# Kernel optimization log

Hardware: AMD Instinct MI355X
Metric: run time of the kernel (lower is better)

Reference implementation:

```python
import jax, jax.numpy as jnp
import numpy as np

CONF_THRESHOLD = 4.0
NMS_THRESHOLD = 0.5
TOP_K = 4096        # fixed candidate cap for jit-static shapes (>> expected #candidates)
NEG = -1.0e9


def setup_inputs() -> dict:
    key = jax.random.key(0)
    k1, k2, k3 = jax.random.split(key, 3)
    B, N, C = 8, 65536, 80
    logits = jax.random.normal(k1, (B, N, C), dtype=jnp.float32)
    # valid xyxy boxes in a ~1000px image: x2>x1, y2>y1
    xy = jax.random.uniform(k2, (B, N, 2), dtype=jnp.float32) * 900.0
    wh = jax.random.uniform(k3, (B, N, 2), dtype=jnp.float32) * 100.0 + 1.0
    boxes = jnp.concatenate([xy, xy + wh], axis=-1)
    return {"logits": logits, "boxes": boxes}


def _pairwise_iou(b):
    # b: [K, 4] xyxy -> [K, K] IoU (torchvision convention, no +1)
    x1, y1, x2, y2 = b[:, 0], b[:, 1], b[:, 2], b[:, 3]
    area = (x2 - x1) * (y2 - y1)                      # [K]
    iw = jnp.maximum(jnp.minimum(x2[:, None], x2[None, :]) - jnp.maximum(x1[:, None], x1[None, :]), 0.0)
    ih = jnp.maximum(jnp.minimum(y2[:, None], y2[None, :]) - jnp.maximum(y1[:, None], y1[None, :]), 0.0)
    inter = iw * ih                                   # [K, K]
    union = area[:, None] + area[None, :] - inter
    return inter / jnp.maximum(union, 1e-12)


def reference(logits, boxes):
    B, N, C = logits.shape
    scores = jnp.max(logits, axis=2)                  # [B, N]
    cls = jnp.argmax(logits, axis=2)                  # [B, N]
    # per-(image, class) NMS category id, as in the torch module
    cat = cls + jnp.arange(B, dtype=cls.dtype)[:, None] * C
    valid = scores > CONF_THRESHOLD                   # [B, N]
    img = jnp.broadcast_to(jnp.arange(B, dtype=jnp.int32)[:, None], (B, N))

    scores_f = scores.reshape(-1)
    valid_f = valid.reshape(-1)
    boxes_f = boxes.reshape(-1, 4)
    cat_f = cat.reshape(-1)
    cls_f = cls.reshape(-1)
    img_f = img.reshape(-1)

    # global descending-score order (matches batched_nms sort); invalid pushed to bottom
    vals, idx = jax.lax.top_k(jnp.where(valid_f, scores_f, NEG), TOP_K)
    bx = boxes_f[idx]                                 # [K, 4]
    ct = cat_f[idx]
    cl = cls_f[idx]
    im = img_f[idx]
    vk = valid_f[idx]                                 # [K]

    iou = _pairwise_iou(bx)                           # [K, K]
    suppress_mat = (ct[:, None] == ct[None, :]) & (iou > NMS_THRESHOLD)
    order = jnp.arange(TOP_K)

    def body(i, keep):
        sup = suppress_mat[i] & (order > i)
        return jnp.where(keep[i], keep & ~sup, keep)

    keep = jax.lax.fori_loop(0, TOP_K, body, vk)      # greedy NMS suppression

    nms_image_idx = jnp.where(keep, im, -1)
    nms_bboxes = bx * keep[:, None].astype(bx.dtype)
    nms_classes = jnp.where(keep, cl, -1)
    nms_scores = jnp.where(keep, vals, 0.0)
    return (nms_image_idx, nms_bboxes, nms_classes, nms_scores)
```

## Files before the change

kernel.cpp:

```cpp
#include <hip/hip_runtime.h>
#include <stdint.h>

typedef unsigned long long u64;
typedef unsigned int u32;
typedef float fv4 __attribute__((ext_vector_type(4)));

#define BATCH  8
#define NPTS   65536
#define NCLS   80
#define NANCH  (BATCH * NPTS)
#define TOPK   4096
#define CONF   4.0f
#define NMSTH  0.5f
#define NCAT   (BATCH * NCLS)
#define BCAP   32

static constexpr size_t OFF_CNT  = 0;
static constexpr size_t OFF_KEYS = 64;

__global__ __launch_bounds__(64) void k_score(const float* __restrict__ logits,
                                              int* __restrict__ cnt,
                                              u64* __restrict__ keys) {
    __shared__ u32 s_sc[64 * 21];
    __shared__ unsigned char s_cl[64 * 20];
    int lane = threadIdx.x;
    const fv4* src = (const fv4*)logits + (size_t)blockIdx.x * 1280;
#pragma unroll
    for (int k = 0; k < 20; ++k) {
        int e = k * 64 + lane;
        fv4 v = __builtin_nontemporal_load(&src[e]);
        float bv = v.x; int bc = 0;
        if (v.y > bv) { bv = v.y; bc = 1; }
        if (v.z > bv) { bv = v.z; bc = 2; }
        if (v.w > bv) { bv = v.w; bc = 3; }
        int a_l = e / 20, j = e % 20;
        u32 eb = __float_as_uint(bv);
        eb = (eb & 0x80000000u) ? ~eb : (eb | 0x80000000u);
        s_sc[a_l * 21 + j] = eb;
        s_cl[a_l * 20 + j] = (unsigned char)(j * 4 + bc);
    }
    __syncthreads();
    u32 best = 0; int bj = 0;
#pragma unroll
    for (int j = 0; j < 20; ++j) {
        u32 p = s_sc[lane * 21 + j];
        if (p > best) { best = p; bj = j; }
    }
    u32 orig = (best & 0x80000000u) ? (best & 0x7fffffffu) : ~best;
    if (__uint_as_float(orig) > CONF) {
        u32 cls = s_cl[lane * 20 + bj];
        u32 a = blockIdx.x * 64 + (u32)lane;
        int pos = atomicAdd(cnt, 1);
        if (pos < 8192)
            keys[pos] = ((u64)best << 32) | ((((~a) & 0x7FFFFu) << 7) | cls);
    }
}

__global__ __launch_bounds__(1024) void k_nms(const int* __restrict__ cnt,
                                              const u64* __restrict__ keys_raw,
                                              const float* __restrict__ boxes,
                                              float* __restrict__ out) {
    __shared__ u64    s_keys[4096];
    __shared__ float4 s_box[4096];
    __shared__ unsigned short s_bucket[NCAT * BCAP];
    __shared__ int s_bcnt[NCAT];
    __shared__ unsigned char s_keep[4096];
    int n = min(*cnt, TOPK);
    int tid = threadIdx.x;
    int n2 = 64; while (n2 < n) n2 <<= 1;

    for (int c = tid; c < NCAT; c += 1024) s_bcnt[c] = 0;
    for (int i = tid; i < n2; i += 1024)
        s_keys[i] = (i < n) ? keys_raw[i] : 0ull;
    __syncthreads();

    for (int k = 2; k <= n2; k <<= 1) {
        for (int j = k >> 1; j > 0; j >>= 1) {
            for (int i = tid; i < n2; i += 1024) {
                int ixj = i ^ j;
                if (ixj > i) {
                    u64 x = s_keys[i], y = s_keys[ixj];
                    bool desc = ((i & k) == 0);
                    if (desc ? (x < y) : (x > y)) { s_keys[i] = y; s_keys[ixj] = x; }
                }
            }
            __syncthreads();
        }
    }

    float4 bx[4]; int cls_[4], img_[4]; float sc_[4];
#pragma unroll
    for (int r = 0; r < 4; ++r) {
        int s = tid + 1024 * r;
        float4 b = make_float4(0.f, 0.f, 0.f, 0.f);
        int cl = -1, im = -1; float v = 0.f;
        if (s < n) {
            u64 key = s_keys[s];
            u32 eb = (u32)(key >> 32);
            u32 orig = (eb & 0x80000000u) ? (eb & 0x7fffffffu) : ~eb;
            v = __uint_as_float(orig);
            u32 low = (u32)key;
            cl = (int)(low & 0x7fu);
            u32 a = (~(low >> 7)) & 0x7FFFFu;
            im = (int)(a >> 16);
            b = ((const float4*)boxes)[a];
            int c = im * NCLS + cl;
            int pos = atomicAdd(&s_bcnt[c], 1);
            if (pos < BCAP) s_bucket[c * BCAP + pos] = (unsigned short)s;
        }
        bx[r] = b; cls_[r] = cl; img_[r] = im; sc_[r] = v;
        s_box[s]  = b;
        s_keep[s] = (s < n) ? 1 : 0;
    }
    __syncthreads();

    if (tid < NCAT) {
        int m = min(s_bcnt[tid], BCAP);
        unsigned short* bkt = &s_bucket[tid * BCAP];
        if (m > 1) {
            for (int i = 1; i < m; ++i) {
                unsigned short x = bkt[i]; int j = i - 1;
                while (j >= 0 && bkt[j] > x) { bkt[j + 1] = bkt[j]; --j; }
                bkt[j + 1] = x;
            }
            for (int i = 1; i < m; ++i) {
                float4 bi = s_box[bkt[i]];
                float areai = (bi.z - bi.x) * (bi.w - bi.y);
                bool dead = false;
                for (int j = 0; j < i && !dead; ++j) {
                    if (!s_keep[bkt[j]]) continue;
                    float4 bj = s_box[bkt[j]];
                    float iw = fmaxf(fminf(bi.z, bj.z) - fmaxf(bi.x, bj.x), 0.f);
                    float ih = fmaxf(fminf(bi.w, bj.w) - fmaxf(bi.y, bj.y), 0.f);
                    float inter = iw * ih;
                    float uni = areai + (bj.z - bj.x) * (bj.w - bj.y) - inter;
                    if (inter / fmaxf(uni, 1e-12f) > NMSTH) dead = true;
                }
                if (dead) s_keep[bkt[i]] = 0;
            }
        }
    }
    __syncthreads();

#pragma unroll
    for (int r = 0; r < 4; ++r) {
        int s = tid + 1024 * r;
        bool keep = s_keep[s] != 0;
        out[s] = keep ? (float)img_[r] : -1.0f;
        ((float4*)(out + 4096))[s] = keep ? bx[r] : make_float4(0.f, 0.f, 0.f, 0.f);
        out[4096 + 16384 + s]        = keep ? (float)cls_[r] : -1.0f;
        out[4096 + 16384 + 4096 + s] = keep ? sc_[r] : 0.0f;
    }
}

extern "C" void kernel_launch(void* const* d_in, const int* in_sizes, int n_in,
                              void* d_out, int out_size, void* d_ws, size_t ws_size,
                              hipStream_t stream) {
    const float* logits = (const float*)d_in[0];
    const float* boxes  = (const float*)d_in[1];
    float* out = (float*)d_out;
    char* ws = (char*)d_ws;

    int* cnt      = (int*)(ws + OFF_CNT);
    u64* keys_raw = (u64*)(ws + OFF_KEYS);

    hipMemsetAsync(cnt, 0, 64, stream);
    k_score<<<NANCH / 64, 64, 0, stream>>>(logits, cnt, keys_raw);
    k_nms<<<1, 1024, 0, stream>>>(cnt, keys_raw, boxes, out);
}
```

Measured before the change: 269.2 us.

## Defer argmax class recovery to NMS kernel and widen score blocks

```diff
diff --git a/kernel.cpp b/kernel.cpp
--- a/kernel.cpp
+++ b/kernel.cpp
@@ -18,46 +18,40 @@
 static constexpr size_t OFF_CNT  = 0;
 static constexpr size_t OFF_KEYS = 64;
 
-__global__ __launch_bounds__(64) void k_score(const float* __restrict__ logits,
-                                              int* __restrict__ cnt,
-                                              u64* __restrict__ keys) {
-    __shared__ u32 s_sc[64 * 21];
-    __shared__ unsigned char s_cl[64 * 20];
-    int lane = threadIdx.x;
-    const fv4* src = (const fv4*)logits + (size_t)blockIdx.x * 1280;
+__global__ __launch_bounds__(256) void k_score(const float* __restrict__ logits,
+                                               int* __restrict__ cnt,
+                                               u64* __restrict__ keys) {
+    __shared__ float s_sc[4][64 * 21];
+    int tid = threadIdx.x;
+    int wid = tid >> 6, lane = tid & 63;
+    int a0 = blockIdx.x * 256 + wid * 64;
+    const fv4* src = (const fv4*)logits + (size_t)a0 * 20;
+    float* reg = s_sc[wid];
 #pragma unroll
     for (int k = 0; k < 20; ++k) {
         int e = k * 64 + lane;
         fv4 v = __builtin_nontemporal_load(&src[e]);
-        float bv = v.x; int bc = 0;
-        if (v.y > bv) { bv = v.y; bc = 1; }
-        if (v.z > bv) { bv = v.z; bc = 2; }
-        if (v.w > bv) { bv = v.w; bc = 3; }
-        int a_l = e / 20, j = e % 20;
-        u32 eb = __float_as_uint(bv);
-        eb = (eb & 0x80000000u) ? ~eb : (eb | 0x80000000u);
-        s_sc[a_l * 21 + j] = eb;
-        s_cl[a_l * 20 + j] = (unsigned char)(j * 4 + bc);
+        float m = fmaxf(fmaxf(v.x, v.y), fmaxf(v.z, v.w));
+        reg[(e / 20) * 21 + (e % 20)] = m;
     }
     __syncthreads();
-    u32 best = 0; int bj = 0;
+    float best = -1e30f;
 #pragma unroll
-    for (int j = 0; j < 20; ++j) {
-        u32 p = s_sc[lane * 21 + j];
-        if (p > best) { best = p; bj = j; }
-    }
-    u32 orig = (best & 0x80000000u) ? (best & 0x7fffffffu) : ~best;
-    if (__uint_as_float(orig) > CONF) {
-        u32 cls = s_cl[lane * 20 + bj];
-        u32 a = blockIdx.x * 64 + (u32)lane;
+    for (int j = 0; j < 20; ++j) best = fmaxf(best, reg[lane * 21 + j]);
+    if (best > CONF) {
         int pos = atomicAdd(cnt, 1);
-        if (pos < 8192)
-            keys[pos] = ((u64)best << 32) | ((((~a) & 0x7FFFFu) << 7) | cls);
+        if (pos < 8192) {
+            u32 eb = __float_as_uint(best);
+            eb = (eb & 0x80000000u) ? ~eb : (eb | 0x80000000u);
+            u32 a = (u32)(a0 + lane);
+            keys[pos] = ((u64)eb << 32) | (u32)(~a);
+        }
     }
 }
 
 __global__ __launch_bounds__(1024) void k_nms(const int* __restrict__ cnt,
                                               const u64* __restrict__ keys_raw,
+                                              const float* __restrict__ logits,
                                               const float* __restrict__ boxes,
                                               float* __restrict__ out) {
     __shared__ u64    s_keys[4096];
@@ -99,10 +93,19 @@
             u32 eb = (u32)(key >> 32);
             u32 orig = (eb & 0x80000000u) ? (eb & 0x7fffffffu) : ~eb;
             v = __uint_as_float(orig);
-            u32 low = (u32)key;
-            cl = (int)(low & 0x7fu);
-            u32 a = (~(low >> 7)) & 0x7FFFFu;
+            u32 a = ~(u32)key;
             im = (int)(a >> 16);
+            const fv4* lp = (const fv4*)logits + (size_t)a * 20;
+            float bv = -1e30f; int bc = 0;
+#pragma unroll
+            for (int k = 0; k < 20; ++k) {
+                fv4 lv = lp[k];
+                if (lv.x > bv) { bv = lv.x; bc = 4 * k; }
+                if (lv.y > bv) { bv = lv.y; bc = 4 * k + 1; }
+                if (lv.z > bv) { bv = lv.z; bc = 4 * k + 2; }
+                if (lv.w > bv) { bv = lv.w; bc = 4 * k + 3; }
+            }
+            cl = bc;
             b = ((const float4*)boxes)[a];
             int c = im * NCLS + cl;
             int pos = atomicAdd(&s_bcnt[c], 1);
@@ -165,6 +168,6 @@
     u64* keys_raw = (u64*)(ws + OFF_KEYS);
 
     hipMemsetAsync(cnt, 0, 64, stream);
-    k_score<<<NANCH / 64, 64, 0, stream>>>(logits, cnt, keys_raw);
-    k_nms<<<1, 1024, 0, stream>>>(cnt, keys_raw, boxes, out);
+    k_score<<<NANCH / 256, 256, 0, stream>>>(logits, cnt, keys_raw);
+    k_nms<<<1, 1024, 0, stream>>>(cnt, keys_raw, logits, boxes, out);
 }
```

Result: slower. 285.6 us (+6.1%).
